# Kernel optimization log

Measured on AMD Instinct MI355X. Metric: run time of the kernel, lower is better.

The kernel has to match this reference:

```python
import jax, jax.numpy as jnp
import numpy as np

IN_F = 4096
OUT_F = 11008
GROUPSIZE = 128
N_GROUPS = IN_F // GROUPSIZE  # 32


def setup_inputs() -> dict:
    key = jax.random.key(0)
    k1, k2, k3, k4 = jax.random.split(key, 4)
    x = jax.random.normal(k1, (4, 2048, IN_F), dtype=jnp.float32)
    # packed 4-bit weights: 8 nibbles per int32 along the input dim
    qweight = jax.random.randint(k2, (IN_F // 8, OUT_F), 0, 2**31 - 1, dtype=jnp.int32)
    # packed 4-bit zero points: 8 nibbles per int32 along the output dim
    qzeros = jax.random.randint(k3, (N_GROUPS, OUT_F // 8), 0, 2**31 - 1, dtype=jnp.int32)
    scales = jax.random.uniform(k4, (N_GROUPS, OUT_F), dtype=jnp.float32,
                                minval=0.001, maxval=0.01)
    g_idx = (jnp.arange(IN_F, dtype=jnp.int32) // GROUPSIZE).astype(jnp.int32)
    return {"x": x, "qweight": qweight, "scales": scales,
            "qzeros": qzeros, "g_idx": g_idx}


def _dequantize(qweight, scales, qzeros, g_idx):
    """GPTQ v2 dequant: W[i, j] = scales[g_idx[i], j] * (q[i, j] - (z[g_idx[i], j] + 1))."""
    shifts = jnp.arange(8, dtype=jnp.int32) * 4  # nibble shift amounts
    # unpack weights along input dim: [in/8, 8, out] -> [in, out]
    q = (qweight[:, None, :] >> shifts[None, :, None]) & 0xF
    q = q.reshape(-1, qweight.shape[1]).astype(scales.dtype)
    # unpack zeros along output dim: [g, out/8, 8] -> [g, out]; +1 per GPTQ v2
    z = ((qzeros[:, :, None] >> shifts[None, None, :]) & 0xF) + 1
    z = z.reshape(qzeros.shape[0], -1).astype(scales.dtype)
    return scales[g_idx] * (q - z[g_idx])  # [in, out]


def reference(x, qweight, scales, qzeros, g_idx):
    W = _dequantize(qweight, scales, qzeros, g_idx)  # [IN_F, OUT_F]
    return jnp.einsum('bsi,io->bso', x, W)
```

## Files before the change

### kernel.cpp

```cpp
#include <hip/hip_runtime.h>
#include <hip/hip_bf16.h>

#define IN_F 4096
#define OUT_F 11008

typedef __bf16 bf16_t;
typedef bf16_t bf16x8 __attribute__((ext_vector_type(8)));
typedef float f32x4 __attribute__((ext_vector_type(4)));
typedef unsigned int u32;

__global__ __launch_bounds__(256) void cvt_x_kernel(const float* __restrict__ x,
                                                    bf16_t* __restrict__ xb) {
    size_t i = ((size_t)blockIdx.x * 256 + threadIdx.x) * 8;
    f32x4 v0 = *(const f32x4*)(x + i);
    f32x4 v1 = *(const f32x4*)(x + i + 4);
    bf16x8 h;
    h[0]=(bf16_t)v0[0]; h[1]=(bf16_t)v0[1]; h[2]=(bf16_t)v0[2]; h[3]=(bf16_t)v0[3];
    h[4]=(bf16_t)v1[0]; h[5]=(bf16_t)v1[1]; h[6]=(bf16_t)v1[2]; h[7]=(bf16_t)v1[3];
    *(bf16x8*)(xb + i) = h;
}

__global__ __launch_bounds__(256) void dequant_kernel(const int* __restrict__ qweight,
                                                      const float* __restrict__ scales,
                                                      const int* __restrict__ qzeros,
                                                      bf16_t* __restrict__ wt) {
    const int n   = blockIdx.x * 256 + threadIdx.x;
    const int kw0 = blockIdx.y * 4;
    const int g   = kw0 >> 4;
    const float s  = scales[(size_t)g * OUT_F + n];
    const int   zw = qzeros[(size_t)g * (OUT_F / 8) + (n >> 3)];
    const float nsz = -s * (float)(((zw >> ((n & 7) * 4)) & 0xF) + 1);
    bf16_t* dst = wt + (size_t)n * IN_F + kw0 * 8;
    #pragma unroll
    for (int j = 0; j < 4; ++j) {
        const int w = qweight[(size_t)(kw0 + j) * OUT_F + n];
        bf16x8 h;
        #pragma unroll
        for (int b = 0; b < 8; ++b)
            h[b] = (bf16_t)fmaf((float)((w >> (4 * b)) & 0xF), s, nsz);
        *(bf16x8*)(dst + j * 8) = h;
    }
}


#define NI (IN_F / 128)

__global__ __launch_bounds__(512, 2) void gemm_8ph(const bf16_t* __restrict__ A,
                                                   const bf16_t* __restrict__ B,
                                                   float* __restrict__ C) {
    __shared__ __align__(16) bf16_t smemA[2 * 2 * 128 * 64];
    __shared__ __align__(16) bf16_t smemB[2 * 2 * 128 * 64];

    const int tid  = threadIdx.x;
    const int lane = tid & 63;
    const int wid  = tid >> 6;
    const int wr   = wid >> 2;
    const int wc   = wid & 3;

    const int bid = blockIdx.x;
    const int swz = (bid & 7) * 172 + (bid >> 3);
    const int bx = swz % 43;
    const int by = swz / 43;
    const int m0 = by * 256;
    const int n0 = bx * 256;

    int lr0, kb0, lr1, kb1;
    {
        int L0 = tid * 16;
        int p0 = L0 ^ (((L0 >> 7) & 7) << 4);
        lr0 = p0 >> 7; kb0 = (p0 & 127) >> 1;
        int L1 = (512 + tid) * 16;
        int p1 = L1 ^ (((L1 >> 7) & 7) << 4);
        lr1 = p1 >> 7; kb1 = (p1 & 127) >> 1;
    }

    const int xm = (lane & 7) << 4;
    const int arow = lane & 15;
    int colk[2];
    #pragma unroll
    for (int ks = 0; ks < 2; ++ks)
        colk[ks] = ((ks * 64) + ((lane >> 4) * 16)) ^ xm;

#define STAGE(smem, buf, half, src, rbase, koff)                                           \
    do {                                                                                   \
        const bf16_t* g0_ = (src) + (size_t)((rbase) + lr0) * IN_F + (koff) + kb0;         \
        __builtin_amdgcn_global_load_lds(                                                  \
            (const __attribute__((address_space(1))) u32*)g0_,                             \
            (__attribute__((address_space(3))) u32*)((char*)(smem) + (buf) * 32768 +       \
                                                     (half) * 16384 + wid * 1024),         \
            16, 0, 0);                                                                     \
        const bf16_t* g1_ = (src) + (size_t)((rbase) + lr1) * IN_F + (koff) + kb1;         \
        __builtin_amdgcn_global_load_lds(                                                  \
            (const __attribute__((address_space(1))) u32*)g1_,                             \
            (__attribute__((address_space(3))) u32*)((char*)(smem) + (buf) * 32768 +       \
                                                     (half) * 16384 + 8192 + wid * 1024),  \
            16, 0, 0);                                                                     \
    } while (0)

#define STAGE_A(buf, half, koff) STAGE(smemA, buf, half, A, m0 + (half) * 128, koff)
#define STAGE_B(buf, half, koff) STAGE(smemB, buf, half, B, n0 + (half) * 128, koff)

#define LOAD_A_FRAGS(dst, buf, mbase)                                                      \
    _Pragma("unroll") for (int mm = 0; mm < 4; ++mm)                                       \
    _Pragma("unroll") for (int ks = 0; ks < 2; ++ks)                                       \
        dst[mm * 2 + ks] = *(const bf16x8*)((const char*)smemA + (buf) * 32768 +           \
            wr * 16384 + (((mbase) + mm) * 16 + arow) * 128 + colk[ks]);

#define LOAD_B_PAIR(dst, buf, P)                                                           \
    _Pragma("unroll") for (int nn = 0; nn < 2; ++nn)                                       \
    _Pragma("unroll") for (int ks = 0; ks < 2; ++ks)                                       \
        dst[nn * 2 + ks] = *(const bf16x8*)((const char*)smemB + (buf) * 32768 +           \
            (wc >> 1) * 16384 + ((wc & 1) * 64 + ((P) * 2 + nn) * 16 + arow) * 128 +       \
            colk[ks]);

#define MFMA_Q(aArr, bArr, mbase, nbase)                                                   \
    __builtin_amdgcn_s_setprio(1);                                                         \
    _Pragma("unroll") for (int mm = 0; mm < 4; ++mm)                                       \
    _Pragma("unroll") for (int nn = 0; nn < 2; ++nn)                                       \
    _Pragma("unroll") for (int ks = 0; ks < 2; ++ks)                                       \
        acc[(mbase) + mm][(nbase) + nn] = __builtin_amdgcn_mfma_f32_16x16x32_bf16(         \
            aArr[mm * 2 + ks], bArr[nn * 2 + ks], acc[(mbase) + mm][(nbase) + nn],         \
            0, 0, 0);                                                                      \
    __builtin_amdgcn_s_setprio(0);

#define BAR() __builtin_amdgcn_s_barrier()
#define LGKM0()                                                                            \
    do {                                                                                   \
        asm volatile("s_waitcnt lgkmcnt(0)" ::: "memory");                                 \
        __builtin_amdgcn_sched_barrier(0);                                                 \
    } while (0)
#define LGKM8() asm volatile("s_waitcnt lgkmcnt(8)" ::: "memory")
#define VMCNT6() asm volatile("s_waitcnt vmcnt(6)" ::: "memory")
#define VMCNT0() asm volatile("s_waitcnt vmcnt(0)" ::: "memory")

    f32x4 acc[8][4];
    #pragma unroll
    for (int m = 0; m < 8; ++m)
        #pragma unroll
        for (int n = 0; n < 4; ++n)
            acc[m][n] = (f32x4)0.0f;

    bf16x8 aR[8], b01[4], b23[4];

    STAGE_B(0, 0, 0);  STAGE_B(0, 1, 0);
    STAGE_A(0, 0, 0);  STAGE_A(0, 1, 0);
    STAGE_B(1, 0, 64); STAGE_B(1, 1, 64);
    STAGE_A(1, 0, 64);
    VMCNT6();
    BAR();

    for (int i = 0; i < NI; ++i) {
        const int  kc = i * 128;
        const int  kn = kc + 128;
        const bool nl = (i + 1 < NI);

        LOAD_A_FRAGS(aR, 0, 0);
        LOAD_B_PAIR(b01, 0, 0);
        STAGE_A(1, 1, kc + 64);
        LGKM8();
        BAR();
        LGKM0();
        MFMA_Q(aR, b01, 0, 0);
        BAR();
        LOAD_B_PAIR(b23, 0, 1);
        if (nl) STAGE_B(0, 0, kn);
        BAR();
        LGKM0();
        MFMA_Q(aR, b23, 0, 2);
        BAR();
        LOAD_A_FRAGS(aR, 0, 4);
        if (nl) STAGE_B(0, 1, kn);
        BAR();
        LGKM0();
        MFMA_Q(aR, b01, 4, 0);
        BAR();
        if (nl) STAGE_A(0, 0, kn);
        BAR();
        MFMA_Q(aR, b23, 4, 2);
        if (nl) VMCNT6(); else VMCNT0();
        BAR();
        LOAD_A_FRAGS(aR, 1, 0);
        LOAD_B_PAIR(b01, 1, 0);
        if (nl) STAGE_A(0, 1, kn);
        LGKM8();
        BAR();
        LGKM0();
        MFMA_Q(aR, b01, 0, 0);
        BAR();
        LOAD_B_PAIR(b23, 1, 1);
        if (nl) STAGE_B(1, 0, kc + 192);
        BAR();
        LGKM0();
        MFMA_Q(aR, b23, 0, 2);
        BAR();
        LOAD_A_FRAGS(aR, 1, 4);
        if (nl) STAGE_B(1, 1, kc + 192);
        BAR();
        LGKM0();
        MFMA_Q(aR, b01, 4, 0);
        BAR();
        if (nl) STAGE_A(1, 0, kc + 192);
        BAR();
        MFMA_Q(aR, b23, 4, 2);
        if (nl) VMCNT6();
        BAR();
    }

    const int cn  = lane & 15;
    const int cr4 = (lane >> 4) * 4;
    #pragma unroll
    for (int m = 0; m < 8; ++m) {
        #pragma unroll
        for (int r = 0; r < 4; ++r) {
            const int grow = m0 + wr * 128 + m * 16 + cr4 + r;
            float* orow = C + (size_t)grow * OUT_F + n0 + wc * 64 + cn;
            #pragma unroll
            for (int n = 0; n < 4; ++n)
                orow[n * 16] = acc[m][n][r];
        }
    }
}

#define BMf 128
#define BNf 128
#define BKf 32
#define LDPF 40

__global__ __launch_bounds__(256, 2) void gptq_gemm_fused(
    const float* __restrict__ x, const int* __restrict__ qweight,
    const float* __restrict__ scales, const int* __restrict__ qzeros,
    float* __restrict__ out)
{
    __shared__ bf16_t As[BMf * LDPF];
    __shared__ bf16_t Bs[BNf * LDPF];
    const int tid = threadIdx.x, lane = tid & 63, wid = tid >> 6;
    const int wr = wid >> 1, wc = wid & 1;
    const int m0 = blockIdx.y * BMf, n0 = blockIdx.x * BNf;
    const int a_row = tid >> 2, a_slot = tid & 3;
    const int b_k8l = tid >> 7, b_n = tid & 127;

    f32x4 acc[4][4];
    #pragma unroll
    for (int i = 0; i < 4; ++i)
        #pragma unroll
        for (int j = 0; j < 4; ++j) acc[i][j] = (f32x4)0.0f;

    for (int kt = 0; kt < IN_F / BKf; ++kt) {
        const int k0 = kt * BKf;
        const int g  = k0 >> 7;
        __syncthreads();
        #pragma unroll
        for (int p = 0; p < 2; ++p) {
            const int row = a_row + p * 64;
            const float* src = x + (size_t)(m0 + row) * IN_F + k0 + a_slot * 8;
            f32x4 v0 = *(const f32x4*)src;
            f32x4 v1 = *(const f32x4*)(src + 4);
            bf16x8 h;
            h[0]=(bf16_t)v0[0]; h[1]=(bf16_t)v0[1]; h[2]=(bf16_t)v0[2]; h[3]=(bf16_t)v0[3];
            h[4]=(bf16_t)v1[0]; h[5]=(bf16_t)v1[1]; h[6]=(bf16_t)v1[2]; h[7]=(bf16_t)v1[3];
            *(bf16x8*)(&As[row * LDPF + a_slot * 8]) = h;
        }
        {
            const int gn = n0 + b_n;
            const float s  = scales[(size_t)g * OUT_F + gn];
            const int   zw = qzeros[(size_t)g * (OUT_F / 8) + (gn >> 3)];
            const float sz = s * (float)(((zw >> ((gn & 7) * 4)) & 0xF) + 1);
            #pragma unroll
            for (int p = 0; p < 2; ++p) {
                const int k8l = b_k8l + p * 2;
                const int w = qweight[(size_t)(k0 / 8 + k8l) * OUT_F + gn];
                bf16x8 h;
                #pragma unroll
                for (int j = 0; j < 8; ++j)
                    h[j] = (bf16_t)fmaf((float)((w >> (4 * j)) & 0xF), s, -sz);
                *(bf16x8*)(&Bs[b_n * LDPF + k8l * 8]) = h;
            }
        }
        __syncthreads();
        bf16x8 af[4], bfr[4];
        #pragma unroll
        for (int m = 0; m < 4; ++m)
            af[m] = *(const bf16x8*)(&As[(wr * 64 + m * 16 + (lane & 15)) * LDPF + (lane >> 4) * 8]);
        #pragma unroll
        for (int n = 0; n < 4; ++n)
            bfr[n] = *(const bf16x8*)(&Bs[(wc * 64 + n * 16 + (lane & 15)) * LDPF + (lane >> 4) * 8]);
        #pragma unroll
        for (int m = 0; m < 4; ++m)
            #pragma unroll
            for (int n = 0; n < 4; ++n)
                acc[m][n] = __builtin_amdgcn_mfma_f32_16x16x32_bf16(af[m], bfr[n], acc[m][n], 0, 0, 0);
    }
    const int cn = lane & 15, cr4 = (lane >> 4) * 4;
    #pragma unroll
    for (int m = 0; m < 4; ++m)
        #pragma unroll
        for (int r = 0; r < 4; ++r) {
            const int grow = m0 + wr * 64 + m * 16 + cr4 + r;
            float* orow = out + (size_t)grow * OUT_F + n0 + wc * 64 + cn;
            #pragma unroll
            for (int n = 0; n < 4; ++n) orow[n * 16] = acc[m][n][r];
        }
}

extern "C" void kernel_launch(void* const* d_in, const int* in_sizes, int n_in,
                              void* d_out, int out_size, void* d_ws, size_t ws_size,
                              hipStream_t stream) {
    const float* x       = (const float*)d_in[0];
    const int*   qweight = (const int*)d_in[1];
    const float* scales  = (const float*)d_in[2];
    const int*   qzeros  = (const int*)d_in[3];
    float* out = (float*)d_out;

    const int M = in_sizes[0] / IN_F;
    const size_t xb_bytes = (size_t)M * IN_F * 2;
    const size_t wt_bytes = (size_t)IN_F * OUT_F * 2;

    if (ws_size >= xb_bytes + wt_bytes && (M % 256) == 0) {
        bf16_t* xb = (bf16_t*)d_ws;
        bf16_t* wt = (bf16_t*)((char*)d_ws + xb_bytes);
        cvt_x_kernel<<<dim3((M * IN_F) / (256 * 8)), dim3(256), 0, stream>>>(x, xb);
        dequant_kernel<<<dim3(OUT_F / 256, IN_F / 32), dim3(256), 0, stream>>>(
            qweight, scales, qzeros, wt);
        const int nwg = (OUT_F / 256) * (M / 256);
        gemm_8ph<<<dim3(nwg), dim3(512), 0, stream>>>(xb, wt, out);
    } else {
        gptq_gemm_fused<<<dim3(OUT_F / BNf, M / BMf), dim3(256), 0, stream>>>(
            x, qweight, scales, qzeros, out);
    }
}
```

Measured before the change: 868.4 us.

## Remove LDS waitcnts and half the barriers, reorder global staging in GEMM loop

Rewrites the main K-loop schedule of the bf16 MFMA GEMM. It drops the explicit lgkmcnt waits and sched barriers, removes roughly half of the workgroup barriers, and moves several global-to-LDS stage operations to different phases, with the vmcnt threshold changed from 6 to 4. The aim is less synchronisation stall and more overlap between MFMA and memory traffic. Without explicit LDS waits the compiler must insert them itself, and with fewer barriers some LDS buffers could be overwritten while other waves are still reading them.

```diff
diff --git a/kernel.cpp b/kernel.cpp
--- a/kernel.cpp
+++ b/kernel.cpp
@@ -124,13 +124,8 @@
     __builtin_amdgcn_s_setprio(0);
 
 #define BAR() __builtin_amdgcn_s_barrier()
-#define LGKM0()                                                                            \
-    do {                                                                                   \
-        asm volatile("s_waitcnt lgkmcnt(0)" ::: "memory");                                 \
-        __builtin_amdgcn_sched_barrier(0);                                                 \
-    } while (0)
-#define LGKM8() asm volatile("s_waitcnt lgkmcnt(8)" ::: "memory")
 #define VMCNT6() asm volatile("s_waitcnt vmcnt(6)" ::: "memory")
+#define VMCNT4() asm volatile("s_waitcnt vmcnt(4)" ::: "memory")
 #define VMCNT0() asm volatile("s_waitcnt vmcnt(0)" ::: "memory")
 
     f32x4 acc[8][4];
@@ -142,8 +137,8 @@
 
     bf16x8 aR[8], b01[4], b23[4];
 
+    STAGE_A(0, 0, 0);  STAGE_A(0, 1, 0);
     STAGE_B(0, 0, 0);  STAGE_B(0, 1, 0);
-    STAGE_A(0, 0, 0);  STAGE_A(0, 1, 0);
     STAGE_B(1, 0, 64); STAGE_B(1, 1, 64);
     STAGE_A(1, 0, 64);
     VMCNT6();
@@ -157,50 +152,33 @@
         LOAD_A_FRAGS(aR, 0, 0);
         LOAD_B_PAIR(b01, 0, 0);
         STAGE_A(1, 1, kc + 64);
-        LGKM8();
-        BAR();
-        LGKM0();
         MFMA_Q(aR, b01, 0, 0);
         BAR();
         LOAD_B_PAIR(b23, 0, 1);
+        MFMA_Q(aR, b23, 0, 2);
+        BAR();
+        LOAD_A_FRAGS(aR, 0, 4);
         if (nl) STAGE_B(0, 0, kn);
-        BAR();
-        LGKM0();
-        MFMA_Q(aR, b23, 0, 2);
-        BAR();
-        LOAD_A_FRAGS(aR, 0, 4);
-        if (nl) STAGE_B(0, 1, kn);
-        BAR();
-        LGKM0();
         MFMA_Q(aR, b01, 4, 0);
         BAR();
         if (nl) STAGE_A(0, 0, kn);
-        BAR();
         MFMA_Q(aR, b23, 4, 2);
-        if (nl) VMCNT6(); else VMCNT0();
+        if (nl) VMCNT4(); else VMCNT0();
         BAR();
         LOAD_A_FRAGS(aR, 1, 0);
         LOAD_B_PAIR(b01, 1, 0);
         if (nl) STAGE_A(0, 1, kn);
-        LGKM8();
-        BAR();
-        LGKM0();
         MFMA_Q(aR, b01, 0, 0);
         BAR();
         LOAD_B_PAIR(b23, 1, 1);
-        if (nl) STAGE_B(1, 0, kc + 192);
-        BAR();
-        LGKM0();
+        if (nl) STAGE_B(0, 1, kn);
         MFMA_Q(aR, b23, 0, 2);
         BAR();
         LOAD_A_FRAGS(aR, 1, 4);
-        if (nl) STAGE_B(1, 1, kc + 192);
-        BAR();
-        LGKM0();
+        if (nl) STAGE_B(1, 0, kn + 64);
         MFMA_Q(aR, b01, 4, 0);
         BAR();
-        if (nl) STAGE_A(1, 0, kc + 192);
-        BAR();
+        if (nl) { STAGE_B(1, 1, kn + 64); STAGE_A(1, 0, kn + 64); }
         MFMA_Q(aR, b23, 4, 2);
         if (nl) VMCNT6();
         BAR();
```

Result: faster. 834.5 us (-3.9%).
